# Kernel optimization log

Hardware: AMD Instinct MI355X
Metric: run time of the kernel (lower is better)

The kernel has to match this reference:

```python
import jax, jax.numpy as jnp
import numpy as np

# Geometry constants replicating odl.tomo.parallel_beam_geometry for a
# 128x128 image on [-20,20]^2 (dx = 40/128 = 0.3125).
N_IMG = 128
EXTENT = 40.0
DX = EXTENT / N_IMG                      # 0.3125
RHO = 20.0 * np.sqrt(2.0)                # max corner radius ~= 28.284
N_ANG = 285                              # ceil(omega * rho), omega = pi/DX
N_DET = 183                              # 2*ceil(rho*omega/pi) + 1
N_T = 384                                # samples along each ray (~dx/1.2 step)
DT = 2.0 * RHO / N_T                     # integration step


def _sample_index_coords():
    """Pixel-index coordinates of all ray sample points.

    Returns float32 array [2, N_ANG, N_DET, N_T]: fractional indices into the
    image for bilinear interpolation. Rays for angle theta travel along
    d = (cos t, sin t); the detector axis is u = (-sin t, cos t).
    """
    ang = (np.arange(N_ANG) + 0.5) * np.pi / N_ANG          # cell centers on [0, pi)
    s = -RHO + (np.arange(N_DET) + 0.5) * (2.0 * RHO / N_DET)
    t = -RHO + (np.arange(N_T) + 0.5) * DT
    cos = np.cos(ang)[:, None, None]
    sin = np.sin(ang)[:, None, None]
    ss = s[None, :, None]
    tt = t[None, None, :]
    px = -ss * sin + tt * cos                               # physical x
    py = ss * cos + tt * sin                                # physical y
    i0 = (px + 20.0) / DX - 0.5                             # fractional row index
    i1 = (py + 20.0) / DX - 0.5                             # fractional col index
    return jnp.asarray(np.stack([i0, i1]), dtype=jnp.float32)


_COORDS = _sample_index_coords()


def setup_inputs() -> dict:
    key = jax.random.key(0)
    x = jax.random.normal(key, (8, N_IMG, N_IMG), dtype=jnp.float32)
    return {"x": x}


def reference(x):
    """Parallel-beam Radon forward projection of x/12 -> sinogram [B, 285, 183]."""
    xs = x / 12.0

    def project_one(img):
        # Bilinear gather at every (angle, det, ray-sample) point, zero outside.
        vals = jax.scipy.ndimage.map_coordinates(
            img, [_COORDS[0], _COORDS[1]], order=1, mode='constant', cval=0.0)
        # Line integral: sum along the ray * step size.
        return vals.sum(axis=-1) * DT                        # [N_ANG, N_DET]

    return jax.vmap(project_one)(xs)
```

## Files before the change

### kernel.cpp

```cpp
#include <hip/hip_runtime.h>
#include <stdint.h>

#define NI 128
#define NA 285
#define ND 183
#define NT 384
#define RAYS (NA * ND)
#define PITCH 133
#define PROWS 132
#define PLDS (PROWS * PITCH)
#define TPB 832
#define NTASK 828
#define IDXM 17420

typedef __fp16 half2v __attribute__((ext_vector_type(2)));

constexpr float PI_F  = 3.14159265358979323846f;
constexpr float RHO_F = 28.284271247461902f;
constexpr float DX_F  = 0.3125f;
constexpr float DT_F  = 2.0f * RHO_F / NT;

__global__ __launch_bounds__(TPB) void radon_fwd(const float* __restrict__ x,
                                                 float* __restrict__ out) {
    __shared__ __align__(16) unsigned int P[PLDS];
    const int tid   = threadIdx.x;
    const int img   = blockIdx.x >> 6;
    const int chunk = blockIdx.x & 63;

    uint4* P4 = (uint4*)P;
    for (int i = tid; i < PLDS / 4; i += TPB) P4[i] = make_uint4(0, 0, 0, 0);
    __syncthreads();

    const float4* src = (const float4*)(x + img * NI * NI);
    for (int i = tid; i < 129 * 32; i += TPB) {
        int pr  = 1 + (i >> 5);
        int g   = i & 31;
        int rlo = pr - 2;
        int rhi = pr - 1;
        float4 vlo = (rlo >= 0)   ? src[rlo * 32 + g] : make_float4(0, 0, 0, 0);
        float4 vhi = (rhi <= 127) ? src[rhi * 32 + g] : make_float4(0, 0, 0, 0);
        int base = pr * PITCH + 2 + g * 4;
        P[base + 0] = __builtin_bit_cast(unsigned int, __builtin_amdgcn_cvt_pkrtz(vlo.x, vhi.x));
        P[base + 1] = __builtin_bit_cast(unsigned int, __builtin_amdgcn_cvt_pkrtz(vlo.y, vhi.y));
        P[base + 2] = __builtin_bit_cast(unsigned int, __builtin_amdgcn_cvt_pkrtz(vlo.z, vhi.z));
        P[base + 3] = __builtin_bit_cast(unsigned int, __builtin_amdgcn_cvt_pkrtz(vlo.w, vhi.w));
    }
    __syncthreads();

    const int w_id = tid >> 6;
    const int lane = tid & 63;
    const int t    = w_id * 64 + chunk;
    const int j    = t / 9;
    const int apc  = t - j * 9;
    const int ap   = apc * 16 + (lane >> 2);
    const int q    = lane & 3;
    const bool valid = (t < NTASK) && (ap < 143);

    const float ang = ((float)ap + 0.5f) * (PI_F / (float)NA);
    float sn, cs;
    sincosf(ang, &sn, &cs);
    const float s   = -RHO_F + ((float)j + 0.5f) * (2.0f * RHO_F / (float)ND);
    const float t0v = -RHO_F + 0.5f * DT_F;
    const float inv_dx = 1.0f / DX_F;

    const float e0 = -s * sn;
    const float e1 =  s * cs;
    const float c0p = (e0 + t0v * cs + 20.0f) * inv_dx + 1.5f;
    const float c1p = (e1 + t0v * sn + 20.0f) * inv_dx + 1.5f;
    const float st0 = DT_F * cs * inv_dx;
    const float st1 = DT_F * sn * inv_dx;

    const float LIM = 20.157f;
    const float inv_cs = 1.0f / cs;
    const float inv_sn = 1.0f / sn;
    float ta = (-LIM - e0) * inv_cs, tb = (LIM - e0) * inv_cs;
    float tc = (-LIM - e1) * inv_sn, td = (LIM - e1) * inv_sn;
    float tlo = fmaxf(fminf(ta, tb), fminf(tc, td));
    float thi = fminf(fmaxf(ta, tb), fmaxf(tc, td));

    const float inv_dt = 1.0f / DT_F;
    float fk0 = fminf(fmaxf(ceilf((tlo - t0v) * inv_dt), 0.0f), 384.0f);
    float fk1 = fminf(fmaxf(floorf((thi - t0v) * inv_dt), -1.0f), 383.0f);
    const int kmin = (int)fk0;
    const int kmax = (int)fk1;
    const int kmid = (kmin + kmax + 1) >> 1;
    const int kql  = (kmin + kmid) >> 1;
    const int kqu  = (kmid + kmax + 1) >> 1;

    int l0 = kmid - kql, l1 = kql - kmin, l2 = kqu - kmid, l3 = kmax - kqu + 1;
    int len = (q & 2) ? ((q & 1) ? l3 : l2) : ((q & 1) ? l1 : l0);
    int ks  = (q & 2) ? ((q & 1) ? kqu : kmid) : ((q & 1) ? (kql - 1) : (kmid - 1));
    if (!valid) len = 0;
    len = max(len, 0);
    const float sgn  = (q & 2) ? 1.0f : -1.0f;
    const float st0s = st0 * sgn;
    const float st1s = st1 * sgn;
    float i0 = fmaf((float)ks, st0, c0p);
    float i1 = fmaf((float)ks, st1, c1p);

    float acc0 = 0.0f, acc1 = 0.0f, acc2 = 0.0f, acc3 = 0.0f;

    #pragma unroll 2
    for (int m = 0; m < len; ++m) {
        float f0 = floorf(i0);
        float f1 = floorf(i1);
        float a0 = i0 - f0;
        float a1 = i1 - f1;
        int f1i = (int)f1;
        int idx = (int)fmaf(f0, 133.0f, f1);
        i0 += st0s;
        i1 += st1s;
        int idx1 = IDXM - idx;
        int idx2 = (idx + 130) - (f1i << 1);
        int idx3 = IDXM - idx2;
        unsigned int u0 = P[idx],  u1 = P[idx + 1];
        unsigned int m0 = P[idx1], m1 = P[idx1 + 1];
        unsigned int r0 = P[idx2], r1 = P[idx2 + 1];
        unsigned int s0 = P[idx3], s1 = P[idx3 + 1];
        half2v w  = __builtin_amdgcn_cvt_pkrtz(1.0f - a0, a0);
        half2v hA = __builtin_amdgcn_cvt_pkrtz(1.0f - a1, 1.0f - a1);
        half2v hB = __builtin_amdgcn_cvt_pkrtz(a1, a1);
        half2v wA = w * hA;
        half2v wB = w * hB;
        unsigned int wAu = __builtin_bit_cast(unsigned int, wA);
        unsigned int wBu = __builtin_bit_cast(unsigned int, wB);
        half2v wmA = __builtin_bit_cast(half2v, __builtin_amdgcn_alignbit(wAu, wAu, 16));
        half2v wmB = __builtin_bit_cast(half2v, __builtin_amdgcn_alignbit(wBu, wBu, 16));
        acc0 = __builtin_amdgcn_fdot2(__builtin_bit_cast(half2v, u0), wA, acc0, false);
        acc0 = __builtin_amdgcn_fdot2(__builtin_bit_cast(half2v, u1), wB, acc0, false);
        acc1 = __builtin_amdgcn_fdot2(__builtin_bit_cast(half2v, m0), wmB, acc1, false);
        acc1 = __builtin_amdgcn_fdot2(__builtin_bit_cast(half2v, m1), wmA, acc1, false);
        acc2 = __builtin_amdgcn_fdot2(__builtin_bit_cast(half2v, r0), wB, acc2, false);
        acc2 = __builtin_amdgcn_fdot2(__builtin_bit_cast(half2v, r1), wA, acc2, false);
        acc3 = __builtin_amdgcn_fdot2(__builtin_bit_cast(half2v, s0), wmA, acc3, false);
        acc3 = __builtin_amdgcn_fdot2(__builtin_bit_cast(half2v, s1), wmB, acc3, false);
    }

    acc0 += __shfl_xor(acc0, 1, 64); acc0 += __shfl_xor(acc0, 2, 64);
    acc1 += __shfl_xor(acc1, 1, 64); acc1 += __shfl_xor(acc1, 2, 64);
    acc2 += __shfl_xor(acc2, 1, 64); acc2 += __shfl_xor(acc2, 2, 64);
    acc3 += __shfl_xor(acc3, 1, 64); acc3 += __shfl_xor(acc3, 2, 64);

    if (valid) {
        float v = (q == 0) ? acc0 : (q == 1) ? acc1 : (q == 2) ? acc2 : acc3;
        int ao  = (q & 2) ? (284 - ap) : ap;
        int det = (q & 1) ? (182 - j) : j;
        out[img * RAYS + ao * ND + det] = v * (DT_F / 12.0f);
    }
}

extern "C" void kernel_launch(void* const* d_in, const int* in_sizes, int n_in,
                              void* d_out, int out_size, void* d_ws, size_t ws_size,
                              hipStream_t stream) {
    const float* x = (const float*)d_in[0];
    float* out = (float*)d_out;
    const int B = in_sizes[0] / (NI * NI);
    dim3 grid(B * 64);
    radon_fwd<<<grid, TPB, 0, stream>>>(x, out);
}
```

Before: 86.30 us.

## Use uniform wave trip count with clamped coordinates and interleaved ray halves

Each ray half is now split into interleaved even and odd samples across lanes with a stride of two, replacing the earlier four-way contiguous quarter split. Every lane loops to the wave-wide maximum length, and the coordinates are clamped into a zero-padded border, so out-of-range samples read zeros instead of needing per-lane bounds. The aim is to remove divergent loop exits and allow deeper unrolling. The full LDS zero-fill is also replaced by zeroing only the border cells. The cost is extra clamp work and wasted iterations for lanes with shorter rays, and it relies on the padding being zero.

Result: faster. 84.48 us (-2.1%).

```diff
diff --git a/kernel.cpp b/kernel.cpp
--- a/kernel.cpp
+++ b/kernel.cpp
@@ -8,7 +8,7 @@
 #define RAYS (NA * ND)
 #define PITCH 133
 #define PROWS 132
-#define PLDS (PROWS * PITCH)
+#define PLDS (PROWS * PITCH + 1)
 #define TPB 832
 #define NTASK 828
 #define IDXM 17420
@@ -27,9 +27,16 @@
     const int img   = blockIdx.x >> 6;
     const int chunk = blockIdx.x & 63;
 
-    uint4* P4 = (uint4*)P;
-    for (int i = tid; i < PLDS / 4; i += TPB) P4[i] = make_uint4(0, 0, 0, 0);
-    __syncthreads();
+    for (int i = tid; i < 1432; i += TPB) {
+        int r, c;
+        if (i < 399) { r = (i < 133) ? 0 : (i < 266 ? 130 : 131);
+                       c = i - ((i < 133) ? 0 : (i < 266 ? 133 : 266)); }
+        else { int k = i - 399; r = 1 + (k >> 3);
+               const int map[8] = {0, 1, 130, 131, 132, 0, 1, 130};
+               c = map[k & 7]; }
+        P[r * PITCH + c] = 0;
+    }
+    if (tid == 0) P[PLDS - 1] = 0;
 
     const float4* src = (const float4*)(x + img * NI * NI);
     for (int i = tid; i < 129 * 32; i += TPB) {
@@ -84,32 +91,40 @@
     const int kmin = (int)fk0;
     const int kmax = (int)fk1;
     const int kmid = (kmin + kmax + 1) >> 1;
-    const int kql  = (kmin + kmid) >> 1;
-    const int kqu  = (kmid + kmax + 1) >> 1;
 
-    int l0 = kmid - kql, l1 = kql - kmin, l2 = kqu - kmid, l3 = kmax - kqu + 1;
-    int len = (q & 2) ? ((q & 1) ? l3 : l2) : ((q & 1) ? l1 : l0);
-    int ks  = (q & 2) ? ((q & 1) ? kqu : kmid) : ((q & 1) ? (kql - 1) : (kmid - 1));
-    if (!valid) len = 0;
-    len = max(len, 0);
-    const float sgn  = (q & 2) ? 1.0f : -1.0f;
-    const float st0s = st0 * sgn;
-    const float st1s = st1 * sgn;
+    int ldown = kmid - kmin;
+    int lup   = kmax - kmid + 1;
+    int mylen = (max(max(ldown, lup), 0) + 1) >> 1;
+    if (!valid) mylen = 0;
+
+    int Lw = mylen;
+    #pragma unroll
+    for (int off = 32; off >= 1; off >>= 1)
+        Lw = max(Lw, __shfl_xor(Lw, off, 64));
+
+    const int h = q >> 1;
+    const int p = q & 1;
+    const float sgn  = h ? 1.0f : -1.0f;
+    const float st0s = st0 * (2.0f * sgn);
+    const float st1s = st1 * (2.0f * sgn);
+    const int   ks   = h ? (kmid + p) : (kmid - 1 - p);
     float i0 = fmaf((float)ks, st0, c0p);
     float i1 = fmaf((float)ks, st1, c1p);
 
     float acc0 = 0.0f, acc1 = 0.0f, acc2 = 0.0f, acc3 = 0.0f;
 
-    #pragma unroll 2
-    for (int m = 0; m < len; ++m) {
-        float f0 = floorf(i0);
-        float f1 = floorf(i1);
-        float a0 = i0 - f0;
-        float a1 = i1 - f1;
+    #pragma unroll 4
+    for (int m = 0; m < Lw; ++m) {
+        float q0 = fminf(fmaxf(i0, 0.5f), 130.49f);
+        float q1 = fminf(fmaxf(i1, 0.5f), 130.49f);
+        i0 += st0s;
+        i1 += st1s;
+        float f0 = floorf(q0);
+        float f1 = floorf(q1);
+        float a0 = q0 - f0;
+        float a1 = q1 - f1;
         int f1i = (int)f1;
         int idx = (int)fmaf(f0, 133.0f, f1);
-        i0 += st0s;
-        i1 += st1s;
         int idx1 = IDXM - idx;
         int idx2 = (idx + 130) - (f1i << 1);
         int idx3 = IDXM - idx2;
```
